# Performance work log

Measured on AMD Instinct MI355X. Metric: run time of the kernel, lower is better.

The kernel has to match this reference:

```python
import jax, jax.numpy as jnp
import numpy as np

N_NODES = 100000
N_EDGES = 3200000
N_GRAPHS = 64
F_IN = 16
HID = 64


def gcn_conv(x, W, b, src, dst, ew, n_nodes):
    """PyG GCNConv with add_self_loops=True, symmetric normalization.
    x' = D^{-1/2} (A + I) D^{-1/2} (x W) + b, self-loop weight 1."""
    h = x @ W                                             # [N, out]
    deg = jax.ops.segment_sum(ew, dst, num_segments=n_nodes) + 1.0  # self-loop adds 1
    dinv = jax.lax.rsqrt(jnp.maximum(deg, 1e-12))         # deg_inv_sqrt
    norm = dinv[src] * ew * dinv[dst]                     # [E]
    agg = jax.ops.segment_sum(h[src] * norm[:, None], dst, num_segments=n_nodes)
    agg = agg + h * (dinv * dinv)[:, None]                # self-loop term
    return agg + b


def setup_inputs() -> dict:
    key = jax.random.key(0)
    ks = jax.random.split(key, 12)
    x = jax.random.normal(ks[0], (N_NODES, F_IN), dtype=jnp.float32)
    edge_index = jax.random.randint(ks[1], (2, N_EDGES), 0, N_NODES, dtype=jnp.int64)
    edge_weight = jax.random.uniform(ks[2], (N_EDGES,), dtype=jnp.float32)
    batch = jnp.sort(jax.random.randint(ks[3], (N_NODES,), 0, N_GRAPHS, dtype=jnp.int64))
    # GCN layer params (PyG lin: x @ W with W [in, out])
    s1 = 1.0 / np.sqrt(F_IN)
    s2 = 1.0 / np.sqrt(HID)
    W1 = jax.random.uniform(ks[4], (F_IN, HID), jnp.float32, -s1, s1)
    b1 = jnp.zeros((HID,), jnp.float32)
    W2 = jax.random.uniform(ks[5], (HID, HID), jnp.float32, -s2, s2)
    b2 = jnp.zeros((HID,), jnp.float32)
    W3 = jax.random.uniform(ks[6], (HID, HID), jnp.float32, -s2, s2)
    b3 = jnp.zeros((HID,), jnp.float32)
    Wout = jax.random.uniform(ks[7], (HID, 1), jnp.float32, -s2, s2)
    bout = jax.random.uniform(ks[8], (1,), jnp.float32, -s2, s2)
    return {"x": x, "edge_index": edge_index, "edge_weight": edge_weight,
            "batch": batch, "W1": W1, "b1": b1, "W2": W2, "b2": b2,
            "W3": W3, "b3": b3, "Wout": Wout, "bout": bout}


def reference(x, edge_index, edge_weight, batch, W1, b1, W2, b2, W3, b3, Wout, bout):
    src, dst = edge_index[0], edge_index[1]
    n = x.shape[0]
    # layer 1
    h = gcn_conv(x, W1, b1, src, dst, edge_weight, n)
    # layer 2: sigmoid -> (dropout p=0 identity) -> GCNConv
    h = gcn_conv(jax.nn.sigmoid(h), W2, b2, src, dst, edge_weight, n)
    # layer 3
    h = gcn_conv(jax.nn.sigmoid(h), W3, b3, src, dst, edge_weight, n)
    # global mean pool over graphs
    sums = jax.ops.segment_sum(h, batch, num_segments=N_GRAPHS)          # [G, HID]
    counts = jax.ops.segment_sum(jnp.ones((n,), h.dtype), batch, num_segments=N_GRAPHS)
    pooled = sums / jnp.maximum(counts, 1.0)[:, None]
    # final linear head (dropout p=0 identity)
    return pooled @ Wout + bout                                          # [G, 1]
```

## Files before the change

kernel.cpp:

```cpp
#include <hip/hip_runtime.h>
#include <hip/hip_bf16.h>

#define HID 64
#define P_BLOCKS 1024
#define MAXB 512
#define BCAP 9216
#define TILE 3200

typedef float v2f __attribute__((ext_vector_type(2)));
typedef unsigned u2v __attribute__((ext_vector_type(2)));

__device__ inline v2f fp8x2_lo(unsigned u) { return __builtin_amdgcn_cvt_pk_f32_fp8(u, false); }
__device__ inline v2f fp8x2_hi(unsigned u) { return __builtin_amdgcn_cvt_pk_f32_fp8(u, true); }

#define GSCALE 16.0f
#define GINV 0.0625f
#define GS1 12.0f
#define GI1 (1.0f / 12.0f)
#define GS2 24.0f
#define GI2 (1.0f / 24.0f)
#define WQINV (1.0f / 4095.0f)

__global__ __launch_bounds__(256) void kp1a_hist(const int* __restrict__ dst,
                                                 int* __restrict__ ghist,
                                                 int nE, int B, int chunk) {
    __shared__ int h[MAXB];
    for (int b = threadIdx.x; b < B; b += 256) h[b] = 0;
    __syncthreads();
    int lo = blockIdx.x * chunk;
    int hi = min(nE, lo + chunk);
    for (int i = lo + threadIdx.x; i < hi; i += 256)
        atomicAdd(&h[dst[i] >> 8], 1);
    __syncthreads();
    for (int b = threadIdx.x; b < B; b += 256)
        ghist[(size_t)b * P_BLOCKS + blockIdx.x] = h[b];
}

__global__ __launch_bounds__(256) void kp1b1_scan(const int* __restrict__ ghist,
                                                  int* __restrict__ goff,
                                                  int* __restrict__ btot) {
    __shared__ int wsum[4];
    __shared__ int woff[4];
    int tid = threadIdx.x;
    int lane = tid & 63, wv = tid >> 6;
    int b = blockIdx.x;
    int4 v = ((const int4*)(ghist + (size_t)b * P_BLOCKS))[tid];
    int s = v.x + v.y + v.z + v.w;
    int sc = s;
#pragma unroll
    for (int off = 1; off < 64; off <<= 1) {
        int t = __shfl_up(sc, off);
        if (lane >= off) sc += t;
    }
    if (lane == 63) wsum[wv] = sc;
    __syncthreads();
    if (tid == 0) {
        int acc = 0;
#pragma unroll
        for (int w = 0; w < 4; ++w) { woff[w] = acc; acc += wsum[w]; }
        btot[b] = acc;
    }
    __syncthreads();
    int ex = woff[wv] + sc - s;
    int4 o;
    o.x = ex;
    o.y = ex + v.x;
    o.z = o.y + v.y;
    o.w = o.z + v.z;
    ((int4*)(goff + (size_t)b * P_BLOCKS))[tid] = o;
}

__global__ __launch_bounds__(512) void kp1b2_scan(const int* __restrict__ btot,
                                                  int* __restrict__ bstart, int B) {
    __shared__ int wsum[8];
    __shared__ int woff[8];
    int tid = threadIdx.x;
    int lane = tid & 63, wv = tid >> 6;
    int tot = (tid < B) ? btot[tid] : 0;
    int sc = tot;
#pragma unroll
    for (int off = 1; off < 64; off <<= 1) {
        int t = __shfl_up(sc, off);
        if (lane >= off) sc += t;
    }
    if (lane == 63) wsum[wv] = sc;
    __syncthreads();
    if (tid == 0) {
        int acc = 0;
#pragma unroll
        for (int w = 0; w < 8; ++w) { woff[w] = acc; acc += wsum[w]; }
        bstart[B] = acc;
    }
    __syncthreads();
    if (tid < B) bstart[tid] = woff[wv] + sc - tot;
}

__global__ __launch_bounds__(256) void kp1c_sort(const int* __restrict__ src,
                                                 const int* __restrict__ dst,
                                                 const float* __restrict__ ew,
                                                 const int* __restrict__ goff,
                                                 const int* __restrict__ bstart,
                                                 int2* __restrict__ bsw,
                                                 int nE, int B, int chunk) {
    __shared__ int2 sorted[TILE];
    __shared__ unsigned short bkt[TILE];
    __shared__ int cnt[MAXB];
    __shared__ int lstart[MAXB];
    __shared__ int lcur[MAXB];
    __shared__ int gcur[MAXB];
    __shared__ int wsum[4];
    __shared__ int woff[4];
    int tid = threadIdx.x;
    int lane = tid & 63, wv = tid >> 6;
    for (int b = tid; b < B; b += 256)
        gcur[b] = bstart[b] + goff[(size_t)b * P_BLOCKS + blockIdx.x];
    int lo = blockIdx.x * chunk;
    int hi = min(nE, lo + chunk);
    for (int tb = lo; tb < hi; tb += TILE) {
        int m = min(hi - tb, TILE);
        cnt[tid] = 0;
        cnt[tid + 256] = 0;
        __syncthreads();
        for (int i = tid; i < m; i += 256)
            atomicAdd(&cnt[dst[tb + i] >> 8], 1);
        __syncthreads();
        int c0 = cnt[2 * tid], c1 = cnt[2 * tid + 1];
        int s = c0 + c1;
        int sc = s;
#pragma unroll
        for (int off = 1; off < 64; off <<= 1) {
            int t = __shfl_up(sc, off);
            if (lane >= off) sc += t;
        }
        if (lane == 63) wsum[wv] = sc;
        __syncthreads();
        if (tid == 0) {
            int acc = 0;
#pragma unroll
            for (int w = 0; w < 4; ++w) { woff[w] = acc; acc += wsum[w]; }
        }
        __syncthreads();
        int ex = woff[wv] + sc - s;
        lstart[2 * tid] = ex;
        lcur[2 * tid] = ex;
        lstart[2 * tid + 1] = ex + c0;
        lcur[2 * tid + 1] = ex + c0;
        __syncthreads();
        for (int i = tid; i < m; i += 256) {
            int d = dst[tb + i];
            int b = d >> 8;
            int pos = atomicAdd(&lcur[b], 1);
            int2 v;
            v.x = src[tb + i] | ((d & 255) << 20);
            v.y = __float_as_int(ew[tb + i]);
            sorted[pos] = v;
            bkt[pos] = (unsigned short)b;
        }
        __syncthreads();
        for (int i = tid; i < m; i += 256) {
            int b = bkt[i];
            bsw[gcur[b] + (i - lstart[b])] = sorted[i];
        }
        __syncthreads();
        for (int b = tid; b < B; b += 256)
            gcur[b] += lcur[b] - lstart[b];
        __syncthreads();
    }
}

__global__ __launch_bounds__(256) void kp2_build(const int2* __restrict__ bsw,
                                                 const int* __restrict__ bstart,
                                                 int* __restrict__ row_start,
                                                 float* __restrict__ dinv,
                                                 unsigned* __restrict__ csr4,
                                                 int n_nodes) {
    __shared__ int2 ebuf[BCAP];
    __shared__ int cnt[256];
    __shared__ float degw[256];
    __shared__ int cur[256];
    __shared__ int wsum[4];
    __shared__ int woff[4];
    int tid = threadIdx.x;
    int lane = tid & 63, wv = tid >> 6;
    int b = blockIdx.x;
    int e0 = bstart[b], e1 = bstart[b + 1];
    int nb = e1 - e0;
    cnt[tid] = 0;
    degw[tid] = 0.0f;
    __syncthreads();
    for (int i = tid; i < nb; i += 256) {
        int2 v = bsw[e0 + i];
        if (i < BCAP) ebuf[i] = v;
        int dlo = (v.x >> 20) & 255;
        atomicAdd(&cnt[dlo], 1);
        atomicAdd(&degw[dlo], __int_as_float(v.y));
    }
    __syncthreads();
    int c = cnt[tid];
    int sc = c;
#pragma unroll
    for (int off = 1; off < 64; off <<= 1) {
        int t = __shfl_up(sc, off);
        if (lane >= off) sc += t;
    }
    if (lane == 63) wsum[wv] = sc;
    __syncthreads();
    if (tid == 0) {
        int acc = 0;
#pragma unroll
        for (int w = 0; w < 4; ++w) { woff[w] = acc; acc += wsum[w]; }
    }
    __syncthreads();
    int ex = woff[wv] + sc - c;
    cur[tid] = ex;
    int node = (b << 8) + tid;
    if (node < n_nodes) {
        row_start[node] = e0 + ex;
        dinv[node] = rsqrtf(fmaxf(degw[tid] + 1.0f, 1e-12f));
    }
    if (b == 0 && tid == 0) row_start[n_nodes] = bstart[gridDim.x];
    __syncthreads();
    for (int i = tid; i < nb; i += 256) {
        int2 v = (i < BCAP) ? ebuf[i] : bsw[e0 + i];
        int dlo = (v.x >> 20) & 255;
        int pos = atomicAdd(&cur[dlo], 1);
        float w = __int_as_float(v.y);
        unsigned wq = (unsigned)(w * 4095.0f + 0.5f);
        csr4[e0 + pos] = ((unsigned)v.x & 0xFFFFFu) | (wq << 20);
    }
}

__global__ __launch_bounds__(256) void k_mm16f4(const float* __restrict__ in,
                                                const float* __restrict__ W,
                                                const float* __restrict__ dinv,
                                                unsigned* __restrict__ gtab,
                                                int n_nodes) {
    __shared__ float Ws[16 * HID];
    for (int i = threadIdx.x; i < 16 * HID; i += 256) Ws[i] = W[i];
    __syncthreads();
    int lane = threadIdx.x & 63;
    int wid = threadIdx.x >> 6;
    int p = lane & 7;
    int q = lane >> 3;
    int nGrp = (n_nodes + 7) >> 3;
    for (int grp = blockIdx.x * 4 + wid; grp < nGrp; grp += gridDim.x * 4) {
        int node = grp * 8 + q;
        bool ok = node < n_nodes;
        float xr0 = ok ? in[node * 16 + p] : 0.0f;
        float xr1 = ok ? in[node * 16 + 8 + p] : 0.0f;
        float di = ok ? dinv[node] : 0.0f;
        v2f a01 = {0.0f, 0.0f}, a23 = {0.0f, 0.0f};
        v2f a45 = {0.0f, 0.0f}, a67 = {0.0f, 0.0f};
#pragma unroll
        for (int k = 0; k < 16; ++k) {
            float xv = __shfl((k < 8) ? xr0 : xr1, q * 8 + (k & 7));
            const float4* wr = (const float4*)&Ws[k * HID + 8 * p];
            float4 w0 = wr[0], w1 = wr[1];
            v2f wl0 = {w0.x, w0.y}, wl1 = {w0.z, w0.w};
            v2f wl2 = {w1.x, w1.y}, wl3 = {w1.z, w1.w};
            a01 += wl0 * xv; a23 += wl1 * xv; a45 += wl2 * xv; a67 += wl3 * xv;
        }
        float sc = di * GS1;
        unsigned pk = __builtin_amdgcn_cvt_scalef32_pk_fp4_f32(0u, a01.x * sc, a01.y * sc, 1.0f, 0);
        pk = __builtin_amdgcn_cvt_scalef32_pk_fp4_f32(pk, a23.x * sc, a23.y * sc, 1.0f, 1);
        pk = __builtin_amdgcn_cvt_scalef32_pk_fp4_f32(pk, a45.x * sc, a45.y * sc, 1.0f, 2);
        pk = __builtin_amdgcn_cvt_scalef32_pk_fp4_f32(pk, a67.x * sc, a67.y * sc, 1.0f, 3);
        if (ok) gtab[(size_t)node * 8 + p] = pk;
    }
}

template <int OUT4>
__global__ __launch_bounds__(256) void k_agg4(const unsigned* __restrict__ g4,
                                              const float* __restrict__ bias,
                                              const float* __restrict__ dinv,
                                              const int* __restrict__ row_start,
                                              const unsigned* __restrict__ csr4,
                                              const float* __restrict__ Wn,
                                              unsigned* __restrict__ outv,
                                              int n_nodes, float ginv_in, float gs_out) {
    __shared__ float Ws[HID * HID];
    __shared__ unsigned esc[4][64];
    for (int i = threadIdx.x; i < HID * HID; i += 256) Ws[i] = Wn[i];
    __syncthreads();
    int lane = threadIdx.x & 63;
    int wid = threadIdx.x >> 6;
    int node = blockIdx.x * 4 + wid;
    if (node >= n_nodes) return;
    int p = lane & 7;
    int q = lane >> 3;

    float diRaw = dinv[node];

    v2f a01 = {0.0f, 0.0f}, a23 = {0.0f, 0.0f};
    v2f a45 = {0.0f, 0.0f}, a67 = {0.0f, 0.0f};
    {
        unsigned su = g4[(size_t)node * 8 + p];
        if (q == 0) {
            a01 = __builtin_amdgcn_cvt_scalef32_pk_f32_fp4(su, 1.0f, 0);
            a23 = __builtin_amdgcn_cvt_scalef32_pk_f32_fp4(su, 1.0f, 1);
            a45 = __builtin_amdgcn_cvt_scalef32_pk_f32_fp4(su, 1.0f, 2);
            a67 = __builtin_amdgcn_cvt_scalef32_pk_f32_fp4(su, 1.0f, 3);
        }
    }
    int e0 = row_start[node], e1 = row_start[node + 1];
    for (int base = e0; base < e1; base += 64) {
        int m = min(64, e1 - base);
        unsigned sw = 0;
        if (lane < m) sw = __builtin_nontemporal_load(csr4 + base + lane);
        esc[wid][lane] = sw;
        int ng8 = (m + 7) >> 3;
        int ng84 = (ng8 + 3) & ~3;
        for (int g0 = 0; g0 < ng84; g0 += 4) {
            unsigned vA = esc[wid][8 * g0 + q];
            unsigned vB = esc[wid][8 * g0 + 8 + q];
            unsigned vC = esc[wid][8 * g0 + 16 + q];
            unsigned vD = esc[wid][8 * g0 + 24 + q];
            unsigned uA = g4[(vA & 0xFFFFFu) * 8u + p];
            unsigned uB = g4[(vB & 0xFFFFFu) * 8u + p];
            unsigned uC = g4[(vC & 0xFFFFFu) * 8u + p];
            unsigned uD = g4[(vD & 0xFFFFFu) * 8u + p];
            float wA = (float)(vA >> 20) * WQINV;
            float wB = (float)(vB >> 20) * WQINV;
            float wC = (float)(vC >> 20) * WQINV;
            float wD = (float)(vD >> 20) * WQINV;
            a01 += __builtin_amdgcn_cvt_scalef32_pk_f32_fp4(uA, 1.0f, 0) * wA;
            a23 += __builtin_amdgcn_cvt_scalef32_pk_f32_fp4(uA, 1.0f, 1) * wA;
            a45 += __builtin_amdgcn_cvt_scalef32_pk_f32_fp4(uA, 1.0f, 2) * wA;
            a67 += __builtin_amdgcn_cvt_scalef32_pk_f32_fp4(uA, 1.0f, 3) * wA;
            a01 += __builtin_amdgcn_cvt_scalef32_pk_f32_fp4(uB, 1.0f, 0) * wB;
            a23 += __builtin_amdgcn_cvt_scalef32_pk_f32_fp4(uB, 1.0f, 1) * wB;
            a45 += __builtin_amdgcn_cvt_scalef32_pk_f32_fp4(uB, 1.0f, 2) * wB;
            a67 += __builtin_amdgcn_cvt_scalef32_pk_f32_fp4(uB, 1.0f, 3) * wB;
            a01 += __builtin_amdgcn_cvt_scalef32_pk_f32_fp4(uC, 1.0f, 0) * wC;
            a23 += __builtin_amdgcn_cvt_scalef32_pk_f32_fp4(uC, 1.0f, 1) * wC;
            a45 += __builtin_amdgcn_cvt_scalef32_pk_f32_fp4(uC, 1.0f, 2) * wC;
            a67 += __builtin_amdgcn_cvt_scalef32_pk_f32_fp4(uC, 1.0f, 3) * wC;
            a01 += __builtin_amdgcn_cvt_scalef32_pk_f32_fp4(uD, 1.0f, 0) * wD;
            a23 += __builtin_amdgcn_cvt_scalef32_pk_f32_fp4(uD, 1.0f, 1) * wD;
            a45 += __builtin_amdgcn_cvt_scalef32_pk_f32_fp4(uD, 1.0f, 2) * wD;
            a67 += __builtin_amdgcn_cvt_scalef32_pk_f32_fp4(uD, 1.0f, 3) * wD;
        }
    }
    float a[8] = {a01.x, a01.y, a23.x, a23.y, a45.x, a45.y, a67.x, a67.y};
#pragma unroll
    for (int i = 0; i < 8; ++i) {
        a[i] += __shfl_xor(a[i], 8);
        a[i] += __shfl_xor(a[i], 16);
        a[i] += __shfl_xor(a[i], 32);
    }
    float di = diRaw * ginv_in;
    float4 bv0 = ((const float4*)bias)[2 * p];
    float4 bv1 = ((const float4*)bias)[2 * p + 1];
    a[0] = fmaf(di, a[0], bv0.x); a[1] = fmaf(di, a[1], bv0.y);
    a[2] = fmaf(di, a[2], bv0.z); a[3] = fmaf(di, a[3], bv0.w);
    a[4] = fmaf(di, a[4], bv1.x); a[5] = fmaf(di, a[5], bv1.y);
    a[6] = fmaf(di, a[6], bv1.z); a[7] = fmaf(di, a[7], bv1.w);
    float s[8];
#pragma unroll
    for (int i = 0; i < 8; ++i) s[i] = 1.0f / (1.0f + __expf(-a[i]));
    v2f o01 = {0.0f, 0.0f}, o23 = {0.0f, 0.0f};
    v2f o45 = {0.0f, 0.0f}, o67 = {0.0f, 0.0f};
#pragma unroll
    for (int st = 0; st < 8; ++st) {
        float av = __shfl(s[st], q);
        const float4* wr = (const float4*)&Ws[(8 * q + st) * HID + 8 * p];
        float4 w0 = wr[0], w1 = wr[1];
        v2f wl0 = {w0.x, w0.y}, wl1 = {w0.z, w0.w};
        v2f wl2 = {w1.x, w1.y}, wl3 = {w1.z, w1.w};
        o01 += wl0 * av; o23 += wl1 * av; o45 += wl2 * av; o67 += wl3 * av;
    }
    float o[8] = {o01.x, o01.y, o23.x, o23.y, o45.x, o45.y, o67.x, o67.y};
#pragma unroll
    for (int i = 0; i < 8; ++i) {
        o[i] += __shfl_xor(o[i], 8);
        o[i] += __shfl_xor(o[i], 16);
        o[i] += __shfl_xor(o[i], 32);
    }
    if (lane < 8) {
        float sc = diRaw * gs_out;
        if (OUT4) {
            unsigned pk = __builtin_amdgcn_cvt_scalef32_pk_fp4_f32(0u, o[0] * sc, o[1] * sc, 1.0f, 0);
            pk = __builtin_amdgcn_cvt_scalef32_pk_fp4_f32(pk, o[2] * sc, o[3] * sc, 1.0f, 1);
            pk = __builtin_amdgcn_cvt_scalef32_pk_fp4_f32(pk, o[4] * sc, o[5] * sc, 1.0f, 2);
            pk = __builtin_amdgcn_cvt_scalef32_pk_fp4_f32(pk, o[6] * sc, o[7] * sc, 1.0f, 3);
            __builtin_nontemporal_store(pk, outv + (size_t)node * 8 + p);
        } else {
            unsigned pk0 = __builtin_amdgcn_cvt_pk_fp8_f32(o[0] * sc, o[1] * sc, 0, false);
            pk0 = __builtin_amdgcn_cvt_pk_fp8_f32(o[2] * sc, o[3] * sc, pk0, true);
            unsigned pk1 = __builtin_amdgcn_cvt_pk_fp8_f32(o[4] * sc, o[5] * sc, 0, false);
            pk1 = __builtin_amdgcn_cvt_pk_fp8_f32(o[6] * sc, o[7] * sc, pk1, true);
            u2v pv; pv.x = pk0; pv.y = pk1;
            __builtin_nontemporal_store(pv, ((u2v*)outv) + (size_t)node * 8 + p);
        }
    }
}

template <int EPI>
__global__ __launch_bounds__(256) void k_aggmm(const unsigned int* __restrict__ g32,
                                               const float* __restrict__ bias,
                                               const float* __restrict__ dinv,
                                               const int* __restrict__ row_start,
                                               const unsigned* __restrict__ csr4,
                                               const float* __restrict__ Wn,
                                               void* __restrict__ outv,
                                               int n_nodes) {
    __shared__ float Ws[(EPI == 1) ? HID * HID : 64];
    __shared__ unsigned esc[4][64];
    if (EPI == 1) {
        for (int i = threadIdx.x; i < HID * HID; i += blockDim.x) Ws[i] = Wn[i];
        __syncthreads();
    }
    int lane = threadIdx.x & 63;
    int wid = threadIdx.x >> 6;
    int node = blockIdx.x * 4 + wid;
    if (node >= n_nodes) return;
    int p = lane & 15;
    int q = lane >> 4;

    float diRaw = dinv[node];
    float4 bv = ((const float4*)bias)[p];

    v2f acc01 = {0.0f, 0.0f}, acc23 = {0.0f, 0.0f};
    {
        unsigned su = g32[node * 16 + p];
        if (q == 0) { acc01 = fp8x2_lo(su); acc23 = fp8x2_hi(su); }
    }
    int e0 = row_start[node], e1 = row_start[node + 1];
    for (int base = e0; base < e1; base += 64) {
        int m = min(64, e1 - base);
        unsigned sw = 0;
        if (lane < m) sw = __builtin_nontemporal_load(csr4 + base + lane);
        esc[wid][lane] = sw;
        int ng = (m + 3) >> 2;
        int ng4 = (ng + 3) & ~3;
        for (int j = 0; j < ng4; j += 4) {
            unsigned vA = esc[wid][4 * j + q];
            unsigned vB = esc[wid][4 * j + 4 + q];
            unsigned vC = esc[wid][4 * j + 8 + q];
            unsigned vD = esc[wid][4 * j + 12 + q];
            unsigned uA = g32[(vA & 0xFFFFFu) * 16u + p];
            unsigned uB = g32[(vB & 0xFFFFFu) * 16u + p];
            unsigned uC = g32[(vC & 0xFFFFFu) * 16u + p];
            unsigned uD = g32[(vD & 0xFFFFFu) * 16u + p];
            float wA = (float)(vA >> 20) * WQINV;
            float wB = (float)(vB >> 20) * WQINV;
            float wC = (float)(vC >> 20) * WQINV;
            float wD = (float)(vD >> 20) * WQINV;
            acc01 += fp8x2_lo(uA) * wA; acc23 += fp8x2_hi(uA) * wA;
            acc01 += fp8x2_lo(uB) * wB; acc23 += fp8x2_hi(uB) * wB;
            acc01 += fp8x2_lo(uC) * wC; acc23 += fp8x2_hi(uC) * wC;
            acc01 += fp8x2_lo(uD) * wD; acc23 += fp8x2_hi(uD) * wD;
        }
    }
    float a0 = acc01.x, a1 = acc01.y, a2 = acc23.x, a3 = acc23.y;
    a0 += __shfl_xor(a0, 16); a0 += __shfl_xor(a0, 32);
    a1 += __shfl_xor(a1, 16); a1 += __shfl_xor(a1, 32);
    a2 += __shfl_xor(a2, 16); a2 += __shfl_xor(a2, 32);
    a3 += __shfl_xor(a3, 16); a3 += __shfl_xor(a3, 32);

    float di = diRaw * GINV;
    a0 = fmaf(di, a0, bv.x);
    a1 = fmaf(di, a1, bv.y);
    a2 = fmaf(di, a2, bv.z);
    a3 = fmaf(di, a3, bv.w);

    if (EPI == 1) {
        float s0 = 1.0f / (1.0f + __expf(-a0));
        float s1 = 1.0f / (1.0f + __expf(-a1));
        float s2 = 1.0f / (1.0f + __expf(-a2));
        float s3 = 1.0f / (1.0f + __expf(-a3));
        float sel = (q == 0) ? s0 : (q == 1) ? s1 : (q == 2) ? s2 : s3;
        int selbase = lane & 48;
        v2f o01 = {0.0f, 0.0f}, o23 = {0.0f, 0.0f};
#pragma unroll
        for (int st = 0; st < 16; ++st) {
            float av = __shfl(sel, selbase + st);
            float4 wv = ((const float4*)Ws)[(4 * st + q) * 16 + p];
            v2f wlo = {wv.x, wv.y}, whi = {wv.z, wv.w};
            o01 += wlo * av;
            o23 += whi * av;
        }
        float o0 = o01.x, o1 = o01.y, o2 = o23.x, o3 = o23.y;
        o0 += __shfl_xor(o0, 16); o0 += __shfl_xor(o0, 32);
        o1 += __shfl_xor(o1, 16); o1 += __shfl_xor(o1, 32);
        o2 += __shfl_xor(o2, 16); o2 += __shfl_xor(o2, 32);
        o3 += __shfl_xor(o3, 16); o3 += __shfl_xor(o3, 32);
        if (lane < 16) {
            float sc = diRaw * GSCALE;
            unsigned pk = __builtin_amdgcn_cvt_pk_fp8_f32(o0 * sc, o1 * sc, 0, false);
            pk = __builtin_amdgcn_cvt_pk_fp8_f32(o2 * sc, o3 * sc, pk, true);
            ((unsigned*)outv)[node * 16 + p] = pk;
        }
    } else {
        float4 wv = ((const float4*)Wn)[p];
        float v = a0 * wv.x + a1 * wv.y + a2 * wv.z + a3 * wv.w;
        v += __shfl_xor(v, 1);
        v += __shfl_xor(v, 2);
        v += __shfl_xor(v, 4);
        v += __shfl_xor(v, 8);
        if (lane == 0) ((float*)outv)[node] = v;
    }
}

__global__ __launch_bounds__(256) void k_poolseg(const float* __restrict__ p,
                                                 const int* __restrict__ batch,
                                                 float* __restrict__ psum,
                                                 float* __restrict__ pcnt,
                                                 int n_nodes) {
    int lane = threadIdx.x & 63;
    int gw = (blockIdx.x * blockDim.x + threadIdx.x) >> 6;
    int node = gw * 64 + lane;
    bool valid = node < n_nodes;
    float v = valid ? p[node] : 0.0f;
    int g = valid ? batch[node] : -1;
    int g0 = __shfl(g, 0);
    if (__all((g == g0) && valid)) {
#pragma unroll
        for (int off = 32; off; off >>= 1) v += __shfl_xor(v, off);
        if (lane == 0) {
            atomicAdd(&psum[g0], v);
            atomicAdd(&pcnt[g0], 64.0f);
        }
    } else if (valid) {
        atomicAdd(&psum[g], v);
        atomicAdd(&pcnt[g], 1.0f);
    }
}

__global__ __launch_bounds__(64) void k_out(const float* __restrict__ psum,
                                            const float* __restrict__ pcnt,
                                            const float* __restrict__ bout,
                                            float* __restrict__ out, int G) {
    int g = threadIdx.x;
    if (g < G) out[g] = psum[g] / fmaxf(pcnt[g], 1.0f) + bout[0];
}

extern "C" void kernel_launch(void* const* d_in, const int* in_sizes, int n_in,
                              void* d_out, int out_size, void* d_ws, size_t ws_size,
                              hipStream_t stream) {
    const float* x    = (const float*)d_in[0];
    const int*   eidx = (const int*)d_in[1];
    const float* ew   = (const float*)d_in[2];
    const int*   batch= (const int*)d_in[3];
    const float* W1   = (const float*)d_in[4];
    const float* b1   = (const float*)d_in[5];
    const float* W2   = (const float*)d_in[6];
    const float* b2   = (const float*)d_in[7];
    const float* W3   = (const float*)d_in[8];
    const float* b3   = (const float*)d_in[9];
    const float* Wout = (const float*)d_in[10];
    const float* bout = (const float*)d_in[11];
    float* out = (float*)d_out;

    const int N = in_sizes[0] / 16;
    const int E = in_sizes[2];
    const int G = out_size;
    const int* src = eidx;
    const int* dst = eidx + E;
    const int B = (N + 255) >> 8;
    const int chunk = (E + P_BLOCKS - 1) / P_BLOCKS;

    size_t off = 0;
    auto carve = [&](size_t bytes) -> void* {
        void* p = (char*)d_ws + off;
        off += (bytes + 255) & ~(size_t)255;
        return p;
    };
    float* psum     = (float*)carve(64 * 4);
    float* pcnt     = (float*)carve(64 * 4);
    size_t zero_bytes = off;
    int*   ghist    = (int*)  carve((size_t)B * P_BLOCKS * 4);
    int*   goff     = (int*)  carve((size_t)B * P_BLOCKS * 4);
    int*   btot     = (int*)  carve((size_t)B * 4);
    int*   bstart   = (int*)  carve((size_t)(B + 1) * 4);
    int2*  bsw      = (int2*) carve((size_t)E * 8);
    int*   row_start= (int*)  carve((size_t)(N + 1) * 4);
    unsigned* csr4  = (unsigned*)carve((size_t)E * 4);
    float* dinv     = (float*)carve((size_t)N * 4);
    unsigned* gA    = (unsigned*)carve((size_t)N * HID);
    unsigned* gB    = (unsigned*)carve((size_t)N * HID);
    float* p        = (float*)carve((size_t)N * 4);
    (void)ws_size;

    (void)hipMemsetAsync(d_ws, 0, zero_bytes, stream);

    const int nodeBlocks = (N + 3) / 4;
    const int waveBlocks = ((N + 63) / 64 * 64 + 255) / 256;
    const int mmB4 = (((N + 7) >> 3) + 3) / 4;

    kp1a_hist<<<P_BLOCKS, 256, 0, stream>>>(dst, ghist, E, B, chunk);
    kp1b1_scan<<<B, 256, 0, stream>>>(ghist, goff, btot);
    kp1b2_scan<<<1, 512, 0, stream>>>(btot, bstart, B);
    kp1c_sort<<<P_BLOCKS, 256, 0, stream>>>(src, dst, ew, goff, bstart,
                                            bsw, E, B, chunk);
    kp2_build<<<B, 256, 0, stream>>>(bsw, bstart, row_start, dinv, csr4, N);

    k_mm16f4<<<mmB4, 256, 0, stream>>>(x, W1, dinv, gA, N);
    k_agg4<1><<<nodeBlocks, 256, 0, stream>>>(gA, b1, dinv, row_start, csr4,
                                              W2, gB, N, GI1, GS2);
    k_agg4<0><<<nodeBlocks, 256, 0, stream>>>(gB, b2, dinv, row_start, csr4,
                                              W3, gA, N, GI2, GSCALE);
    k_aggmm<2><<<nodeBlocks, 256, 0, stream>>>(gA, b3, dinv, row_start, csr4,
                                               Wout, p, N);

    k_poolseg<<<waveBlocks, 256, 0, stream>>>(p, batch, psum, pcnt, N);
    k_out<<<1, 64, 0, stream>>>(psum, pcnt, bout, out, G);
}
```

Baseline: 459.5 us.

## Project layer-3 features onto Wout before aggregation, gather scalars from LDS

Uses linearity to apply the output head (Wout) to the layer-3 input features before the final aggregation. The last edge gather then moves one fp8 scalar per node instead of a 64-wide fp8 row. A new k_dot kernel builds the per-node fp8 scalar table plus a bias constant. A k_agg3t kernel loads the whole 100K-byte table into LDS and does a wave-per-node scalar reduction over the CSR edges. This removes most of the random global gather traffic in the third layer, at the cost of an extra launch, an extra fp8 quantization of the projected scalar, and a large-LDS, low-occupancy kernel capped at NCAP nodes.

```diff
diff --git a/kernel.cpp b/kernel.cpp
--- a/kernel.cpp
+++ b/kernel.cpp
@@ -6,6 +6,7 @@
 #define MAXB 512
 #define BCAP 9216
 #define TILE 3200
+#define NCAP 131072
 
 typedef float v2f __attribute__((ext_vector_type(2)));
 typedef unsigned u2v __attribute__((ext_vector_type(2)));
@@ -395,110 +396,73 @@
     }
 }
 
-template <int EPI>
-__global__ __launch_bounds__(256) void k_aggmm(const unsigned int* __restrict__ g32,
-                                               const float* __restrict__ bias,
-                                               const float* __restrict__ dinv,
-                                               const int* __restrict__ row_start,
-                                               const unsigned* __restrict__ csr4,
-                                               const float* __restrict__ Wn,
-                                               void* __restrict__ outv,
-                                               int n_nodes) {
-    __shared__ float Ws[(EPI == 1) ? HID * HID : 64];
-    __shared__ unsigned esc[4][64];
-    if (EPI == 1) {
-        for (int i = threadIdx.x; i < HID * HID; i += blockDim.x) Ws[i] = Wn[i];
-        __syncthreads();
-    }
+__global__ __launch_bounds__(256) void k_dot(const unsigned* __restrict__ g32,
+                                             const float* __restrict__ Wout,
+                                             const float* __restrict__ b3,
+                                             unsigned char* __restrict__ t8,
+                                             float* __restrict__ c0,
+                                             int n_nodes) {
+    __shared__ float Ws[64];
+    if (threadIdx.x < 64) Ws[threadIdx.x] = Wout[threadIdx.x];
+    __syncthreads();
     int lane = threadIdx.x & 63;
     int wid = threadIdx.x >> 6;
-    int node = blockIdx.x * 4 + wid;
-    if (node >= n_nodes) return;
     int p = lane & 15;
     int q = lane >> 4;
-
-    float diRaw = dinv[node];
-    float4 bv = ((const float4*)bias)[p];
-
-    v2f acc01 = {0.0f, 0.0f}, acc23 = {0.0f, 0.0f};
-    {
-        unsigned su = g32[node * 16 + p];
-        if (q == 0) { acc01 = fp8x2_lo(su); acc23 = fp8x2_hi(su); }
-    }
-    int e0 = row_start[node], e1 = row_start[node + 1];
-    for (int base = e0; base < e1; base += 64) {
-        int m = min(64, e1 - base);
-        unsigned sw = 0;
-        if (lane < m) sw = __builtin_nontemporal_load(csr4 + base + lane);
-        esc[wid][lane] = sw;
-        int ng = (m + 3) >> 2;
-        int ng4 = (ng + 3) & ~3;
-        for (int j = 0; j < ng4; j += 4) {
-            unsigned vA = esc[wid][4 * j + q];
-            unsigned vB = esc[wid][4 * j + 4 + q];
-            unsigned vC = esc[wid][4 * j + 8 + q];
-            unsigned vD = esc[wid][4 * j + 12 + q];
-            unsigned uA = g32[(vA & 0xFFFFFu) * 16u + p];
-            unsigned uB = g32[(vB & 0xFFFFFu) * 16u + p];
-            unsigned uC = g32[(vC & 0xFFFFFu) * 16u + p];
-            unsigned uD = g32[(vD & 0xFFFFFu) * 16u + p];
-            float wA = (float)(vA >> 20) * WQINV;
-            float wB = (float)(vB >> 20) * WQINV;
-            float wC = (float)(vC >> 20) * WQINV;
-            float wD = (float)(vD >> 20) * WQINV;
-            acc01 += fp8x2_lo(uA) * wA; acc23 += fp8x2_hi(uA) * wA;
-            acc01 += fp8x2_lo(uB) * wB; acc23 += fp8x2_hi(uB) * wB;
-            acc01 += fp8x2_lo(uC) * wC; acc23 += fp8x2_hi(uC) * wC;
-            acc01 += fp8x2_lo(uD) * wD; acc23 += fp8x2_hi(uD) * wD;
-        }
-    }
-    float a0 = acc01.x, a1 = acc01.y, a2 = acc23.x, a3 = acc23.y;
-    a0 += __shfl_xor(a0, 16); a0 += __shfl_xor(a0, 32);
-    a1 += __shfl_xor(a1, 16); a1 += __shfl_xor(a1, 32);
-    a2 += __shfl_xor(a2, 16); a2 += __shfl_xor(a2, 32);
-    a3 += __shfl_xor(a3, 16); a3 += __shfl_xor(a3, 32);
-
-    float di = diRaw * GINV;
-    a0 = fmaf(di, a0, bv.x);
-    a1 = fmaf(di, a1, bv.y);
-    a2 = fmaf(di, a2, bv.z);
-    a3 = fmaf(di, a3, bv.w);
-
-    if (EPI == 1) {
-        float s0 = 1.0f / (1.0f + __expf(-a0));
-        float s1 = 1.0f / (1.0f + __expf(-a1));
-        float s2 = 1.0f / (1.0f + __expf(-a2));
-        float s3 = 1.0f / (1.0f + __expf(-a3));
-        float sel = (q == 0) ? s0 : (q == 1) ? s1 : (q == 2) ? s2 : s3;
-        int selbase = lane & 48;
-        v2f o01 = {0.0f, 0.0f}, o23 = {0.0f, 0.0f};
-#pragma unroll
-        for (int st = 0; st < 16; ++st) {
-            float av = __shfl(sel, selbase + st);
-            float4 wv = ((const float4*)Ws)[(4 * st + q) * 16 + p];
-            v2f wlo = {wv.x, wv.y}, whi = {wv.z, wv.w};
-            o01 += wlo * av;
-            o23 += whi * av;
-        }
-        float o0 = o01.x, o1 = o01.y, o2 = o23.x, o3 = o23.y;
-        o0 += __shfl_xor(o0, 16); o0 += __shfl_xor(o0, 32);
-        o1 += __shfl_xor(o1, 16); o1 += __shfl_xor(o1, 32);
-        o2 += __shfl_xor(o2, 16); o2 += __shfl_xor(o2, 32);
-        o3 += __shfl_xor(o3, 16); o3 += __shfl_xor(o3, 32);
-        if (lane < 16) {
-            float sc = diRaw * GSCALE;
-            unsigned pk = __builtin_amdgcn_cvt_pk_fp8_f32(o0 * sc, o1 * sc, 0, false);
-            pk = __builtin_amdgcn_cvt_pk_fp8_f32(o2 * sc, o3 * sc, pk, true);
-            ((unsigned*)outv)[node * 16 + p] = pk;
-        }
-    } else {
-        float4 wv = ((const float4*)Wn)[p];
-        float v = a0 * wv.x + a1 * wv.y + a2 * wv.z + a3 * wv.w;
-        v += __shfl_xor(v, 1);
-        v += __shfl_xor(v, 2);
-        v += __shfl_xor(v, 4);
-        v += __shfl_xor(v, 8);
-        if (lane == 0) ((float*)outv)[node] = v;
+    int node = (blockIdx.x * 4 + wid) * 4 + q;
+    if (blockIdx.x == 0 && threadIdx.x == 0) {
+        float s = 0.0f;
+        for (int f = 0; f < 64; ++f) s += b3[f] * Ws[f];
+        c0[0] = s;
+    }
+    if (node >= n_nodes) return;
+    unsigned u = g32[(size_t)node * 16 + p];
+    v2f lo = fp8x2_lo(u), hi = fp8x2_hi(u);
+    float4 wv = ((const float4*)Ws)[p];
+    float v = lo.x * wv.x + lo.y * wv.y + hi.x * wv.z + hi.y * wv.w;
+    v += __shfl_xor(v, 1);
+    v += __shfl_xor(v, 2);
+    v += __shfl_xor(v, 4);
+    v += __shfl_xor(v, 8);
+    if (p == 0) {
+        unsigned pk = __builtin_amdgcn_cvt_pk_fp8_f32(v, 0.0f, 0, false);
+        t8[node] = (unsigned char)(pk & 0xFFu);
+    }
+}
+
+__global__ __launch_bounds__(1024) void k_agg3t(const unsigned char* __restrict__ t8,
+                                                const int* __restrict__ row_start,
+                                                const float* __restrict__ dinv,
+                                                const unsigned* __restrict__ csr4,
+                                                const float* __restrict__ c0p,
+                                                float* __restrict__ p,
+                                                int n_nodes, int nbPer) {
+    __shared__ unsigned char ts[NCAP];
+    int tid = threadIdx.x;
+    int ndw = (n_nodes + 3) >> 2;
+    const unsigned* t32 = (const unsigned*)t8;
+    for (int i = tid; i < ndw; i += 1024) ((unsigned*)ts)[i] = t32[i];
+    __syncthreads();
+    float c0 = c0p[0];
+    int lane = tid & 63, wid = tid >> 6;
+    int lo = blockIdx.x * nbPer;
+    int hi = min(n_nodes, lo + nbPer);
+    for (int node = lo + wid; node < hi; node += 16) {
+        int e0 = row_start[node], e1 = row_start[node + 1];
+        float acc = 0.0f;
+        for (int base = e0; base < e1; base += 64) {
+            int i = base + lane;
+            unsigned sw = (i < e1) ? csr4[i] : 0u;
+            float tv = fp8x2_lo((unsigned)ts[sw & 0xFFFFFu]).x;
+            acc += (float)(sw >> 20) * tv;
+        }
+        acc *= WQINV;
+#pragma unroll
+        for (int off = 32; off; off >>= 1) acc += __shfl_xor(acc, off);
+        if (lane == 0) {
+            float self = fp8x2_lo((unsigned)ts[node]).x;
+            p[node] = fmaf(dinv[node] * GINV, acc + self, c0);
+        }
     }
 }
 
@@ -580,6 +544,8 @@
     unsigned* gA    = (unsigned*)carve((size_t)N * HID);
     unsigned* gB    = (unsigned*)carve((size_t)N * HID);
     float* p        = (float*)carve((size_t)N * 4);
+    unsigned char* t8 = (unsigned char*)carve((size_t)N + 256);
+    float* c0buf    = (float*)carve(256);
     (void)ws_size;
 
     (void)hipMemsetAsync(d_ws, 0, zero_bytes, stream);
@@ -600,8 +566,9 @@
                                               W2, gB, N, GI1, GS2);
     k_agg4<0><<<nodeBlocks, 256, 0, stream>>>(gB, b2, dinv, row_start, csr4,
                                               W3, gA, N, GI2, GSCALE);
-    k_aggmm<2><<<nodeBlocks, 256, 0, stream>>>(gA, b3, dinv, row_start, csr4,
-                                               Wout, p, N);
+    k_dot<<<(N + 15) / 16, 256, 0, stream>>>(gA, Wout, b3, t8, c0buf, N);
+    k_agg3t<<<256, 1024, 0, stream>>>(t8, row_start, dinv, csr4, c0buf, p, N,
+                                      (N + 255) / 256);
 
     k_poolseg<<<waveBlocks, 256, 0, stream>>>(p, batch, psum, pcnt, N);
     k_out<<<1, 64, 0, stream>>>(psum, pcnt, bout, out, G);
```

Result: no change. 462.6 us (+0.7%).
